# Performance work log

Measured on AMD Instinct MI355X. Metric: run time of the kernel, lower is better.

## Reference

```python
import jax, jax.numpy as jnp
import numpy as np

GRID_MIN, GRID_MAX, NUM_GRIDS = -2.0, 2.0, 8
DENOM = (GRID_MAX - GRID_MIN) / (NUM_GRIDS - 1)
DIM, NUM_HEADS = 768, 12
B, N = 8, 1024


def _layer_norm(x, w, b, eps=1e-5):
    mu = jnp.mean(x, axis=-1, keepdims=True)
    var = jnp.mean((x - mu) ** 2, axis=-1, keepdims=True)
    return (x - mu) * jax.lax.rsqrt(var + eps) * w + b


def _fastkan(x, ln_w, ln_b, spline_w, base_w, base_b):
    # x: [..., C]; spline_w: [C*G, O]; base_w: [C, O]
    grid = jnp.linspace(GRID_MIN, GRID_MAX, NUM_GRIDS, dtype=x.dtype)
    h = _layer_norm(x, ln_w, ln_b)
    # RBF basis expansion: [..., C, G]
    basis = jnp.exp(-(((h[..., None] - grid) / DENOM) ** 2))
    basis = basis.reshape(*basis.shape[:-2], -1)  # [..., C*G]
    ret = basis @ spline_w
    ret = ret + jax.nn.silu(x) @ base_w + base_b
    return ret


def setup_inputs() -> dict:
    key = jax.random.key(0)
    ks = jax.random.split(key, 6)
    C = DIM
    return {
        "x": jax.random.normal(ks[0], (B, N, C), jnp.float32),
        "qkv_ln_w": jnp.ones((C,), jnp.float32),
        "qkv_ln_b": jnp.zeros((C,), jnp.float32),
        "qkv_spline_w": jax.random.normal(ks[1], (C * NUM_GRIDS, 3 * C), jnp.float32) * 0.1,
        "qkv_base_w": jax.random.normal(ks[2], (C, 3 * C), jnp.float32) * (1.0 / np.sqrt(C)),
        "qkv_base_b": jnp.zeros((3 * C,), jnp.float32),
        "proj_ln_w": jnp.ones((C,), jnp.float32),
        "proj_ln_b": jnp.zeros((C,), jnp.float32),
        "proj_spline_w": jax.random.normal(ks[3], (C * NUM_GRIDS, C), jnp.float32) * 0.1,
        "proj_base_w": jax.random.normal(ks[4], (C, C), jnp.float32) * (1.0 / np.sqrt(C)),
        "proj_base_b": jnp.zeros((C,), jnp.float32),
    }


def reference(x, qkv_ln_w, qkv_ln_b, qkv_spline_w, qkv_base_w, qkv_base_b,
              proj_ln_w, proj_ln_b, proj_spline_w, proj_base_w, proj_base_b):
    b, n, c = x.shape
    h = NUM_HEADS
    d = c // h
    scale = d ** -0.5
    qkv = _fastkan(x, qkv_ln_w, qkv_ln_b, qkv_spline_w, qkv_base_w, qkv_base_b)
    qkv = qkv.reshape(b, n, 3, h, d).transpose(2, 0, 3, 1, 4)  # [3,B,H,N,D]
    q, k, v = qkv[0], qkv[1], qkv[2]
    attn = jnp.einsum("bhnd,bhmd->bhnm", q, k) * scale
    attn = jax.nn.softmax(attn, axis=-1)
    out = jnp.einsum("bhnm,bhmd->bhnd", attn, v)
    out = out.transpose(0, 2, 1, 3).reshape(b, n, c)
    out = _fastkan(out, proj_ln_w, proj_ln_b, proj_spline_w, proj_base_w, proj_base_b)
    return out
```

## Files before the change

kernel.cpp:

```cpp
#include <hip/hip_runtime.h>
#include <cstdint>
#include <cstddef>

typedef _Float16 h8 __attribute__((ext_vector_type(8)));
typedef float f4 __attribute__((ext_vector_type(4)));
typedef float f16f __attribute__((ext_vector_type(16)));

#define DEV static __device__ __forceinline__

DEV void gld16(const void* g, void* l) {
  __builtin_amdgcn_global_load_lds(
      (const __attribute__((address_space(1))) void*)g,
      (__attribute__((address_space(3))) void*)l, 16, 0, 0);
}

__global__ __launch_bounds__(256)
void kan_prep(const float* __restrict__ X, const float* __restrict__ lnw,
              const float* __restrict__ lnb, _Float16* __restrict__ Acat) {
  const int row = blockIdx.x;
  const int tid = threadIdx.x;
  const float* xr = X + (size_t)row * 768;
  float xv[3];
  xv[0] = xr[tid]; xv[1] = xr[tid + 256]; xv[2] = xr[tid + 512];
  float s = xv[0] + xv[1] + xv[2];
  float q = xv[0] * xv[0] + xv[1] * xv[1] + xv[2] * xv[2];
#pragma unroll
  for (int off = 32; off; off >>= 1) {
    s += __shfl_xor(s, off);
    q += __shfl_xor(q, off);
  }
  __shared__ float rs_[4], rq_[4];
  const int wave = tid >> 6;
  if ((tid & 63) == 0) { rs_[wave] = s; rq_[wave] = q; }
  __syncthreads();
  s = rs_[0] + rs_[1] + rs_[2] + rs_[3];
  q = rq_[0] + rq_[1] + rq_[2] + rq_[3];
  const float mu = s * (1.0f / 768.0f);
  const float var = q * (1.0f / 768.0f) - mu * mu;
  const float rsig = rsqrtf(var + 1e-5f);
  _Float16* out = Acat + (size_t)row * 6912;
#pragma unroll
  for (int i = 0; i < 3; ++i) {
    const int c = tid + i * 256;
    const float x = xv[i];
    const float h = (x - mu) * rsig * lnw[c] + lnb[c];
    union { h8 v; _Float16 u[8]; } bs;
#pragma unroll
    for (int g = 0; g < 8; ++g) {
      const float gv = -2.0f + (4.0f / 7.0f) * (float)g;
      const float t = (h - gv) * 1.75f;
      bs.u[g] = (_Float16)__expf(-t * t);
    }
    *(h8*)(out + c * 8) = bs.v;
    out[6144 + c] = (_Float16)(x / (1.0f + __expf(-x)));
  }
}

__global__ __launch_bounds__(256)
void wt_cast(const float* __restrict__ W, _Float16* __restrict__ Bp,
             int N, int koff, int nkt) {
  __shared__ float t[32][33];
  const int k0 = blockIdx.x * 32, n0 = blockIdx.y * 32;
  const int tx = threadIdx.x & 31, ty = threadIdx.x >> 5;
#pragma unroll
  for (int i = 0; i < 4; ++i)
    t[ty + i * 8][tx] = W[(size_t)(k0 + ty + i * 8) * N + n0 + tx];
  __syncthreads();
  const int f = threadIdx.x;
  if (f < 128) {
    const int nn = f & 31, cc = f >> 5;
    union { h8 v; _Float16 u[8]; } bs;
#pragma unroll
    for (int j = 0; j < 8; ++j) bs.u[j] = (_Float16)t[cc * 8 + j][nn];
    const int kg = koff + k0 + cc * 8;
    const int nt = (n0 + nn) >> 5;
    const size_t addr = ((size_t)nt * nkt + (kg >> 6)) * 2048 +
                        (size_t)((((kg >> 4) & 3) * 64 + nn + 32 * ((kg >> 3) & 1))) * 8;
    *(h8*)(Bp + addr) = bs.v;
  }
}

__global__ __launch_bounds__(256)
void v_transpose(const _Float16* __restrict__ qkv, _Float16* __restrict__ Vt) {
  const int bh = blockIdx.z, hh = bh % 12, b = bh / 12;
  const int kvb = blockIdx.x * 32, db = blockIdx.y * 32;
  __shared__ _Float16 t[32][33];
  const int tx = threadIdx.x & 31, ty = threadIdx.x >> 5;
#pragma unroll
  for (int i = 0; i < 4; ++i) {
    const int kv = kvb + ty + i * 8;
    t[ty + i * 8][tx] = qkv[(size_t)(b * 1024 + kv) * 2304 + 1536 + hh * 64 + db + tx];
  }
  __syncthreads();
#pragma unroll
  for (int i = 0; i < 4; ++i) {
    const int d = db + ty + i * 8;
    Vt[(size_t)(bh * 64 + d) * 1024 + kvb + tx] = t[tx][ty + i * 8];
  }
}

#define LOAD_B(dst)                                       \
  {                                                       \
    _Pragma("unroll") for (int ni = 0; ni < 2; ++ni) {    \
      _Pragma("unroll") for (int ks = 0; ks < 4; ++ks)    \
        dst[ni][ks] = *(const h8*)(bpp[ni] + ks * 512);   \
      bpp[ni] += 2048;                                    \
    }                                                     \
  }
#define LOAD_A(buf)                                       \
  {                                                       \
    _Pragma("unroll") for (int i = 0; i < 4; ++i) {       \
      gld16(ap[i], (buf) + alOff[i]);                     \
      ap[i] += 64;                                        \
    }                                                     \
  }
#define MFMA_STEP(buf, br)                                \
  {                                                       \
    const h8* A8 = (const h8*)(buf);                      \
    _Pragma("unroll") for (int ks = 0; ks < 4; ++ks) {    \
      const int o = (ks * 2 + half) ^ swz;                \
      h8 af0 = A8[(wm + l31) * 8 + o];                    \
      h8 af1 = A8[(wm + 32 + l31) * 8 + o];               \
      acc[0][0] = __builtin_amdgcn_mfma_f32_32x32x16_f16(af0, br[0][ks], acc[0][0], 0, 0, 0); \
      acc[0][1] = __builtin_amdgcn_mfma_f32_32x32x16_f16(af0, br[1][ks], acc[0][1], 0, 0, 0); \
      acc[1][0] = __builtin_amdgcn_mfma_f32_32x32x16_f16(af1, br[0][ks], acc[1][0], 0, 0, 0); \
      acc[1][1] = __builtin_amdgcn_mfma_f32_32x32x16_f16(af1, br[1][ks], acc[1][1], 0, 0, 0); \
    }                                                     \
  }

template <bool F16OUT>
__global__ __launch_bounds__(256, 2)
void gemm_bt(const _Float16* __restrict__ A, const _Float16* __restrict__ Bp,
             const float* __restrict__ bias, void* __restrict__ Cout,
             int N, int ldK, int kLen, size_t sliceStride) {
  __shared__ __align__(16) _Float16 As[2 * 128 * 64];
  _Float16* As0 = As;
  _Float16* As1 = As + 128 * 64;
  const int tid = threadIdx.x;
  const int lane = tid & 63, wave = tid >> 6;
  const int gx = gridDim.x;
  const int lin = blockIdx.y * gx + blockIdx.x;
  const int xcd = lin & 7, pos = lin >> 3;
  const int bandH = gridDim.y >> 3;
  const int bm = (xcd * bandH + pos / gx) * 128;
  const int bn = (pos % gx) * 128;
  const int slice = blockIdx.z;
  const int kOff = slice * kLen;
  const int rsub = lane >> 3;
  const int l7 = lane & 7;
  const int l31 = lane & 31, half = lane >> 5;
  const int wm = (wave >> 1) * 64, wn = (wave & 1) * 64;
  const _Float16* ap[4];
  int alOff[4];
#pragma unroll
  for (int i = 0; i < 4; ++i) {
    const int ch = wave * 4 + i;
    const int ksw = (l7 ^ rsub ^ ((ch & 3) << 1)) * 8;
    ap[i] = A + (size_t)(bm + ch * 8 + rsub) * ldK + kOff + ksw;
    alOff[i] = ch * 512;
  }
  const size_t nktTot = (size_t)(ldK >> 6);
  const int kt0 = kOff >> 6;
  const _Float16* bpp[2];
#pragma unroll
  for (int ni = 0; ni < 2; ++ni)
    bpp[ni] = Bp + ((size_t)((bn >> 5) + (wn >> 5) + ni) * nktTot + kt0) * 2048 + lane * 8;

  f16f acc[2][2] = {};
  const int swz = l7 ^ ((rsub & 3) << 1);
  const int nkt = kLen >> 6;
  h8 bregA[2][4], bregB[2][4];
  LOAD_B(bregA);
  LOAD_A(As0);
  for (int kt = 0; kt < nkt; kt += 2) {
    __syncthreads();
    if (kt + 1 < nkt) { LOAD_B(bregB); LOAD_A(As1); }
    MFMA_STEP(As0, bregA);
    __syncthreads();
    if (kt + 2 < nkt) { LOAD_B(bregA); LOAD_A(As0); }
    MFMA_STEP(As1, bregB);
  }
#pragma unroll
  for (int ni = 0; ni < 2; ++ni) {
    const int col = bn + wn + ni * 32 + l31;
    const float bv = bias ? bias[col] : 0.0f;
#pragma unroll
    for (int mi = 0; mi < 2; ++mi) {
      const int rb = bm + wm + mi * 32 + 4 * half;
#pragma unroll
      for (int reg = 0; reg < 16; ++reg) {
        const int r = rb + (reg & 3) + 8 * (reg >> 2);
        const float v = acc[mi][ni][reg] + bv;
        if (F16OUT)
          ((_Float16*)Cout)[(size_t)r * N + col] = (_Float16)v;
        else
          ((float*)Cout + slice * sliceStride)[(size_t)r * N + col] = v;
      }
    }
  }
}

__global__ __launch_bounds__(256)
void attn(const _Float16* __restrict__ qkv, const _Float16* __restrict__ Vt,
          float* __restrict__ ctx) {
  __shared__ __align__(16) _Float16 Qs[128 * 64];
  __shared__ __align__(16) _Float16 Ks[64 * 64];
  __shared__ __align__(16) _Float16 Vs[64 * 64];
  __shared__ __align__(16) _Float16 Ps[4 * 32 * 72];
  const int tid = threadIdx.x;
  const int lane = tid & 63, wave = tid >> 6;
  const int bh = blockIdx.y, hh = bh % 12, b = bh / 12;
  const int qt = blockIdx.x;
  const int rsub = lane >> 3;
  const int ksw = ((lane & 7) ^ rsub) * 8;
#pragma unroll
  for (int i = 0; i < 4; ++i) {
    const int ch = wave * 4 + i;
    const int row = ch * 8 + rsub;
    gld16(qkv + (size_t)(b * 1024 + qt * 128 + row) * 2304 + hh * 64 + ksw, Qs + ch * 512);
  }
  const int l16 = lane & 15, quad = lane >> 4, r7 = l16 & 7;
  f4 acc_o[2][4] = {};
  float m_old[2][4], l_sum[2][4];
#pragma unroll
  for (int mi = 0; mi < 2; ++mi)
#pragma unroll
    for (int j = 0; j < 4; ++j) { m_old[mi][j] = -1e30f; l_sum[mi][j] = 0.0f; }

  _Float16* Pw = Ps + wave * (32 * 72);

  for (int kv0 = 0; kv0 < 1024; kv0 += 64) {
#pragma unroll
    for (int i = 0; i < 2; ++i) {
      const int ch = wave * 2 + i;
      const int row = ch * 8 + rsub;
      gld16(qkv + (size_t)(b * 1024 + kv0 + row) * 2304 + 768 + hh * 64 + ksw, Ks + ch * 512);
      gld16(Vt + (size_t)(bh * 64 + row) * 1024 + kv0 + ksw, Vs + ch * 512);
    }
    __syncthreads();
    const h8* Q8 = (const h8*)Qs;
    const h8* K8 = (const h8*)Ks;
    const h8* V8 = (const h8*)Vs;
    f4 s[2][4] = {};
#pragma unroll
    for (int ks = 0; ks < 2; ++ks) {
      const int kq = (ks * 4 + quad) ^ r7;
      h8 qf[2], kf[4];
#pragma unroll
      for (int mi = 0; mi < 2; ++mi) qf[mi] = Q8[(wave * 32 + mi * 16 + l16) * 8 + kq];
#pragma unroll
      for (int ni = 0; ni < 4; ++ni) kf[ni] = K8[(ni * 16 + l16) * 8 + kq];
#pragma unroll
      for (int mi = 0; mi < 2; ++mi)
#pragma unroll
        for (int ni = 0; ni < 4; ++ni)
          s[mi][ni] = __builtin_amdgcn_mfma_f32_16x16x32_f16(qf[mi], kf[ni], s[mi][ni], 0, 0, 0);
    }
#pragma unroll
    for (int mi = 0; mi < 2; ++mi)
#pragma unroll
      for (int ni = 0; ni < 4; ++ni) s[mi][ni] *= 0.125f;
#pragma unroll
    for (int mi = 0; mi < 2; ++mi) {
#pragma unroll
      for (int j = 0; j < 4; ++j) {
        float vm = fmaxf(fmaxf(s[mi][0][j], s[mi][1][j]), fmaxf(s[mi][2][j], s[mi][3][j]));
#pragma unroll
        for (int off = 1; off < 16; off <<= 1) vm = fmaxf(vm, __shfl_xor(vm, off));
        const float mn = fmaxf(m_old[mi][j], vm);
        const float alpha = __expf(m_old[mi][j] - mn);
        float rs = 0.0f;
#pragma unroll
        for (int ni = 0; ni < 4; ++ni) {
          const float p = __expf(s[mi][ni][j] - mn);
          s[mi][ni][j] = p;
          rs += p;
        }
#pragma unroll
        for (int off = 1; off < 16; off <<= 1) rs += __shfl_xor(rs, off);
        l_sum[mi][j] = l_sum[mi][j] * alpha + rs;
        m_old[mi][j] = mn;
#pragma unroll
        for (int ni = 0; ni < 4; ++ni) acc_o[mi][ni][j] *= alpha;
      }
    }
#pragma unroll
    for (int mi = 0; mi < 2; ++mi)
#pragma unroll
      for (int ni = 0; ni < 4; ++ni)
#pragma unroll
        for (int j = 0; j < 4; ++j)
          Pw[(mi * 16 + quad * 4 + j) * 72 + ni * 16 + l16] = (_Float16)s[mi][ni][j];
#pragma unroll
    for (int ks = 0; ks < 2; ++ks) {
      const int kq = ks * 4 + quad;
      h8 pf[2], vf[4];
#pragma unroll
      for (int mi = 0; mi < 2; ++mi) pf[mi] = *(const h8*)(Pw + (mi * 16 + l16) * 72 + kq * 8);
#pragma unroll
      for (int ni = 0; ni < 4; ++ni) vf[ni] = V8[(ni * 16 + l16) * 8 + (kq ^ r7)];
#pragma unroll
      for (int mi = 0; mi < 2; ++mi)
#pragma unroll
        for (int ni = 0; ni < 4; ++ni)
          acc_o[mi][ni] = __builtin_amdgcn_mfma_f32_16x16x32_f16(pf[mi], vf[ni], acc_o[mi][ni], 0, 0, 0);
    }
    __syncthreads();
  }
#pragma unroll
  for (int mi = 0; mi < 2; ++mi) {
#pragma unroll
    for (int j = 0; j < 4; ++j) {
      const float inv = 1.0f / l_sum[mi][j];
      const int tok = b * 1024 + qt * 128 + wave * 32 + mi * 16 + quad * 4 + j;
      float* cr = ctx + (size_t)tok * 768 + hh * 64;
#pragma unroll
      for (int ni = 0; ni < 4; ++ni) cr[ni * 16 + l16] = acc_o[mi][ni][j] * inv;
    }
  }
}

extern "C" void kernel_launch(void* const* d_in, const int* in_sizes, int n_in,
                              void* d_out, int out_size, void* d_ws, size_t ws_size,
                              hipStream_t stream) {
  (void)in_sizes; (void)n_in; (void)out_size; (void)ws_size;
  const float* x    = (const float*)d_in[0];
  const float* qlnw = (const float*)d_in[1];
  const float* qlnb = (const float*)d_in[2];
  const float* qsw  = (const float*)d_in[3];
  const float* qbw  = (const float*)d_in[4];
  const float* qbb  = (const float*)d_in[5];
  const float* plnw = (const float*)d_in[6];
  const float* plnb = (const float*)d_in[7];
  const float* psw  = (const float*)d_in[8];
  const float* pbw  = (const float*)d_in[9];
  const float* pbb  = (const float*)d_in[10];
  float* out = (float*)d_out;

  _Float16* WtQ  = (_Float16*)d_ws;
  _Float16* WtP  = WtQ + (size_t)2304 * 6912;
  _Float16* Acat = WtP + (size_t)768 * 6912;
  _Float16* QKV  = Acat + (size_t)8192 * 6912;
  _Float16* Vt   = QKV + (size_t)8192 * 2304;
  float* CTX = (float*)(Vt + (size_t)96 * 64 * 1024);

  dim3 blk(256);
  wt_cast<<<dim3(192, 72), blk, 0, stream>>>(qsw, WtQ, 2304, 0, 108);
  wt_cast<<<dim3(24, 72),  blk, 0, stream>>>(qbw, WtQ, 2304, 6144, 108);
  wt_cast<<<dim3(192, 24), blk, 0, stream>>>(psw, WtP, 768, 0, 108);
  wt_cast<<<dim3(24, 24),  blk, 0, stream>>>(pbw, WtP, 768, 6144, 108);
  kan_prep<<<8192, blk, 0, stream>>>(x, qlnw, qlnb, Acat);
  gemm_bt<true><<<dim3(2304 / 128, 8192 / 128, 1), blk, 0, stream>>>(
      Acat, WtQ, qbb, QKV, 2304, 6912, 6912, 0);
  v_transpose<<<dim3(32, 2, 96), blk, 0, stream>>>(QKV, Vt);
  attn<<<dim3(8, 96), blk, 0, stream>>>(QKV, Vt, CTX);
  kan_prep<<<8192, blk, 0, stream>>>(CTX, plnw, plnb, Acat);
  gemm_bt<false><<<dim3(768 / 128, 8192 / 128, 1), blk, 0, stream>>>(
      Acat, WtP, pbb, out, 768, 6912, 6912, 0);
}
```

Baseline: 717.0 us.

## Use 256x128 tile GEMM with XCD-aware block mapping for QKV projection

Adds a new GEMM kernel for the QKV KAN projection that computes 256x128 output tiles per block, with 4x2 MFMA tiles per wave, double-buffered A tiles in LDS and B held in registers. Blocks are remapped so each XCD processes a contiguous band of M rows, which is meant to improve L2 reuse of the A and B operands. The larger tile halves B reloads per output and raises arithmetic intensity. The cost is more accumulator registers and 64KB of LDS per block, which may reduce occupancy.

```diff
diff --git a/kernel.cpp b/kernel.cpp
--- a/kernel.cpp
+++ b/kernel.cpp
@@ -200,6 +200,89 @@
   }
 }
 
+__global__ __launch_bounds__(256, 2)
+void gemm_bt2(const _Float16* __restrict__ A, const _Float16* __restrict__ Bp,
+              const float* __restrict__ bias, _Float16* __restrict__ Cout,
+              int N, int ldK) {
+  __shared__ __align__(16) _Float16 As[2 * 256 * 64];
+  _Float16* As0 = As;
+  _Float16* As1 = As + 256 * 64;
+  const int tid = threadIdx.x;
+  const int lane = tid & 63, wave = tid >> 6;
+  const int gx = gridDim.x;
+  const int lin = blockIdx.y * gx + blockIdx.x;
+  const int xcd = lin & 7, pos = lin >> 3;
+  const int bandH = gridDim.y >> 3;
+  const int bm = (xcd * bandH + pos / gx) * 256;
+  const int bn = (pos % gx) * 128;
+  const int rsub = lane >> 3;
+  const int l7 = lane & 7;
+  const int l31 = lane & 31, half = lane >> 5;
+  const int wm = (wave >> 1) * 128, wn = (wave & 1) * 64;
+  const _Float16* ap[8];
+  int alOff[8];
+#pragma unroll
+  for (int i = 0; i < 8; ++i) {
+    const int ch = wave * 8 + i;
+    const int ksw = (l7 ^ rsub ^ ((ch & 3) << 1)) * 8;
+    ap[i] = A + (size_t)(bm + ch * 8 + rsub) * ldK + ksw;
+    alOff[i] = ch * 512;
+  }
+  const size_t nktTot = (size_t)(ldK >> 6);
+  const _Float16* bpp[2];
+#pragma unroll
+  for (int ni = 0; ni < 2; ++ni)
+    bpp[ni] = Bp + (size_t)((bn >> 5) + (wn >> 5) + ni) * nktTot * 2048 + lane * 8;
+
+  f16f acc[4][2] = {};
+  const int swz = l7 ^ ((rsub & 3) << 1);
+  const int nkt = ldK >> 6;
+  h8 bregA[2][4], bregB[2][4];
+#define LOAD_A2(buf)                                      \
+  {                                                       \
+    _Pragma("unroll") for (int i = 0; i < 8; ++i) {       \
+      gld16(ap[i], (buf) + alOff[i]);                     \
+      ap[i] += 64;                                        \
+    }                                                     \
+  }
+#define MFMA_STEP2(buf, br)                               \
+  {                                                       \
+    const h8* A8 = (const h8*)(buf);                      \
+    _Pragma("unroll") for (int ks = 0; ks < 4; ++ks) {    \
+      const int o = (ks * 2 + half) ^ swz;                \
+      _Pragma("unroll") for (int mi = 0; mi < 4; ++mi) {  \
+        h8 af = A8[(wm + mi * 32 + l31) * 8 + o];         \
+        acc[mi][0] = __builtin_amdgcn_mfma_f32_32x32x16_f16(af, br[0][ks], acc[mi][0], 0, 0, 0); \
+        acc[mi][1] = __builtin_amdgcn_mfma_f32_32x32x16_f16(af, br[1][ks], acc[mi][1], 0, 0, 0); \
+      }                                                   \
+    }                                                     \
+  }
+  LOAD_B(bregA);
+  LOAD_A2(As0);
+  for (int kt = 0; kt < nkt; kt += 2) {
+    __syncthreads();
+    if (kt + 1 < nkt) { LOAD_B(bregB); LOAD_A2(As1); }
+    MFMA_STEP2(As0, bregA);
+    __syncthreads();
+    if (kt + 2 < nkt) { LOAD_B(bregA); LOAD_A2(As0); }
+    MFMA_STEP2(As1, bregB);
+  }
+#pragma unroll
+  for (int ni = 0; ni < 2; ++ni) {
+    const int col = bn + wn + ni * 32 + l31;
+    const float bv = bias[col];
+#pragma unroll
+    for (int mi = 0; mi < 4; ++mi) {
+      const int rb = bm + wm + mi * 32 + 4 * half;
+#pragma unroll
+      for (int reg = 0; reg < 16; ++reg) {
+        const int r = rb + (reg & 3) + 8 * (reg >> 2);
+        Cout[(size_t)r * N + col] = (_Float16)(acc[mi][ni][reg] + bv);
+      }
+    }
+  }
+}
+
 __global__ __launch_bounds__(256)
 void attn(const _Float16* __restrict__ qkv, const _Float16* __restrict__ Vt,
           float* __restrict__ ctx) {
@@ -350,8 +433,8 @@
   wt_cast<<<dim3(192, 24), blk, 0, stream>>>(psw, WtP, 768, 0, 108);
   wt_cast<<<dim3(24, 24),  blk, 0, stream>>>(pbw, WtP, 768, 6144, 108);
   kan_prep<<<8192, blk, 0, stream>>>(x, qlnw, qlnb, Acat);
-  gemm_bt<true><<<dim3(2304 / 128, 8192 / 128, 1), blk, 0, stream>>>(
-      Acat, WtQ, qbb, QKV, 2304, 6912, 6912, 0);
+  gemm_bt2<<<dim3(2304 / 128, 8192 / 256), blk, 0, stream>>>(
+      Acat, WtQ, qbb, QKV, 2304, 6912);
   v_transpose<<<dim3(32, 2, 96), blk, 0, stream>>>(QKV, Vt);
   attn<<<dim3(8, 96), blk, 0, stream>>>(QKV, Vt, CTX);
   kan_prep<<<8192, blk, 0, stream>>>(CTX, plnw, plnb, Acat);
```

Result: slower. 733.5 us (+2.3%).

## Enlarge attention KV tile to 128, keep Q in registers, fold scale into exp

Applied to the files above, without the earlier changes.

The attention kernel now loads each wave's Q fragments straight into registers instead of staging them through shared memory. The KV tile grows from 64 to 128 keys per iteration, which halves the number of barrier-synchronised loop trips. The 0.125 scale is folded into the exponent argument, and s_setprio hints are wrapped around the MFMA sections. In exchange the kernel uses more score registers and a new V swizzle layout, which may lower occupancy.

```diff
diff --git a/kernel.cpp b/kernel.cpp
--- a/kernel.cpp
+++ b/kernel.cpp
@@ -203,23 +203,26 @@
 __global__ __launch_bounds__(256)
 void attn(const _Float16* __restrict__ qkv, const _Float16* __restrict__ Vt,
           float* __restrict__ ctx) {
-  __shared__ __align__(16) _Float16 Qs[128 * 64];
-  __shared__ __align__(16) _Float16 Ks[64 * 64];
-  __shared__ __align__(16) _Float16 Vs[64 * 64];
+  __shared__ __align__(16) _Float16 Ks[128 * 64];
+  __shared__ __align__(16) _Float16 Vs[64 * 128];
   __shared__ __align__(16) _Float16 Ps[4 * 32 * 72];
   const int tid = threadIdx.x;
   const int lane = tid & 63, wave = tid >> 6;
   const int bh = blockIdx.y, hh = bh % 12, b = bh / 12;
   const int qt = blockIdx.x;
   const int rsub = lane >> 3;
-  const int ksw = ((lane & 7) ^ rsub) * 8;
-#pragma unroll
-  for (int i = 0; i < 4; ++i) {
-    const int ch = wave * 4 + i;
-    const int row = ch * 8 + rsub;
-    gld16(qkv + (size_t)(b * 1024 + qt * 128 + row) * 2304 + hh * 64 + ksw, Qs + ch * 512);
-  }
+  const int l7 = lane & 7;
+  const int ksw = (l7 ^ rsub) * 8;
   const int l16 = lane & 15, quad = lane >> 4, r7 = l16 & 7;
+  const int l15 = lane & 15, q4 = lane >> 4;
+  h8 qreg[2][2];
+#pragma unroll
+  for (int mi = 0; mi < 2; ++mi)
+#pragma unroll
+    for (int ks = 0; ks < 2; ++ks) {
+      const size_t row = (size_t)(b * 1024 + qt * 128 + wave * 32 + mi * 16 + l16);
+      qreg[mi][ks] = *(const h8*)(qkv + row * 2304 + hh * 64 + (ks * 4 + quad) * 8);
+    }
   f4 acc_o[2][4] = {};
   float m_old[2][4], l_sum[2][4];
 #pragma unroll
@@ -229,50 +232,55 @@
 
   _Float16* Pw = Ps + wave * (32 * 72);
 
-  for (int kv0 = 0; kv0 < 1024; kv0 += 64) {
-#pragma unroll
-    for (int i = 0; i < 2; ++i) {
-      const int ch = wave * 2 + i;
+  for (int it = 0; it < 8; ++it) {
+    const int kv0 = it * 128;
+#pragma unroll
+    for (int i = 0; i < 4; ++i) {
+      const int ch = wave * 4 + i;
       const int row = ch * 8 + rsub;
-      gld16(qkv + (size_t)(b * 1024 + kv0 + row) * 2304 + 768 + hh * 64 + ksw, Ks + ch * 512);
-      gld16(Vt + (size_t)(bh * 64 + row) * 1024 + kv0 + ksw, Vs + ch * 512);
+      gld16(qkv + (size_t)(b * 1024 + kv0 + row) * 2304 + 768 + hh * 64 + ksw,
+            Ks + ch * 512);
+    }
+#pragma unroll
+    for (int i = 0; i < 4; ++i) {
+      const int chv = wave * 4 + i;
+      const int d = chv * 4 + q4;
+      const int csw = l15 ^ (d & 7);
+      gld16(Vt + (size_t)(bh * 64 + d) * 1024 + kv0 + csw * 8, Vs + chv * 512);
     }
     __syncthreads();
-    const h8* Q8 = (const h8*)Qs;
     const h8* K8 = (const h8*)Ks;
     const h8* V8 = (const h8*)Vs;
-    f4 s[2][4] = {};
+    f4 s[2][8] = {};
+    __builtin_amdgcn_s_setprio(1);
 #pragma unroll
     for (int ks = 0; ks < 2; ++ks) {
       const int kq = (ks * 4 + quad) ^ r7;
-      h8 qf[2], kf[4];
-#pragma unroll
-      for (int mi = 0; mi < 2; ++mi) qf[mi] = Q8[(wave * 32 + mi * 16 + l16) * 8 + kq];
-#pragma unroll
-      for (int ni = 0; ni < 4; ++ni) kf[ni] = K8[(ni * 16 + l16) * 8 + kq];
+      h8 kf[8];
+#pragma unroll
+      for (int ni = 0; ni < 8; ++ni) kf[ni] = K8[(ni * 16 + l16) * 8 + kq];
 #pragma unroll
       for (int mi = 0; mi < 2; ++mi)
 #pragma unroll
-        for (int ni = 0; ni < 4; ++ni)
-          s[mi][ni] = __builtin_amdgcn_mfma_f32_16x16x32_f16(qf[mi], kf[ni], s[mi][ni], 0, 0, 0);
-    }
-#pragma unroll
-    for (int mi = 0; mi < 2; ++mi)
-#pragma unroll
-      for (int ni = 0; ni < 4; ++ni) s[mi][ni] *= 0.125f;
+        for (int ni = 0; ni < 8; ++ni)
+          s[mi][ni] = __builtin_amdgcn_mfma_f32_16x16x32_f16(qreg[mi][ks], kf[ni], s[mi][ni], 0, 0, 0);
+    }
+    __builtin_amdgcn_s_setprio(0);
 #pragma unroll
     for (int mi = 0; mi < 2; ++mi) {
 #pragma unroll
       for (int j = 0; j < 4; ++j) {
-        float vm = fmaxf(fmaxf(s[mi][0][j], s[mi][1][j]), fmaxf(s[mi][2][j], s[mi][3][j]));
+        float vm = s[mi][0][j];
+#pragma unroll
+        for (int ni = 1; ni < 8; ++ni) vm = fmaxf(vm, s[mi][ni][j]);
 #pragma unroll
         for (int off = 1; off < 16; off <<= 1) vm = fmaxf(vm, __shfl_xor(vm, off));
         const float mn = fmaxf(m_old[mi][j], vm);
-        const float alpha = __expf(m_old[mi][j] - mn);
+        const float alpha = __expf((m_old[mi][j] - mn) * 0.125f);
         float rs = 0.0f;
 #pragma unroll
-        for (int ni = 0; ni < 4; ++ni) {
-          const float p = __expf(s[mi][ni][j] - mn);
+        for (int ni = 0; ni < 8; ++ni) {
+          const float p = __expf((s[mi][ni][j] - mn) * 0.125f);
           s[mi][ni][j] = p;
           rs += p;
         }
@@ -285,25 +293,33 @@
       }
     }
 #pragma unroll
-    for (int mi = 0; mi < 2; ++mi)
-#pragma unroll
-      for (int ni = 0; ni < 4; ++ni)
-#pragma unroll
-        for (int j = 0; j < 4; ++j)
-          Pw[(mi * 16 + quad * 4 + j) * 72 + ni * 16 + l16] = (_Float16)s[mi][ni][j];
-#pragma unroll
-    for (int ks = 0; ks < 2; ++ks) {
-      const int kq = ks * 4 + quad;
-      h8 pf[2], vf[4];
-#pragma unroll
-      for (int mi = 0; mi < 2; ++mi) pf[mi] = *(const h8*)(Pw + (mi * 16 + l16) * 72 + kq * 8);
-#pragma unroll
-      for (int ni = 0; ni < 4; ++ni) vf[ni] = V8[(ni * 16 + l16) * 8 + (kq ^ r7)];
+    for (int hf = 0; hf < 2; ++hf) {
 #pragma unroll
       for (int mi = 0; mi < 2; ++mi)
 #pragma unroll
         for (int ni = 0; ni < 4; ++ni)
-          acc_o[mi][ni] = __builtin_amdgcn_mfma_f32_16x16x32_f16(pf[mi], vf[ni], acc_o[mi][ni], 0, 0, 0);
+#pragma unroll
+          for (int j = 0; j < 4; ++j)
+            Pw[(mi * 16 + quad * 4 + j) * 72 + ni * 16 + l16] =
+                (_Float16)s[mi][hf * 4 + ni][j];
+      __builtin_amdgcn_s_setprio(1);
+#pragma unroll
+      for (int ks = 0; ks < 2; ++ks) {
+        const int kq = hf * 8 + ks * 4 + quad;
+        h8 pf[2], vf[4];
+#pragma unroll
+        for (int mi = 0; mi < 2; ++mi)
+          pf[mi] = *(const h8*)(Pw + (mi * 16 + l16) * 72 + (ks * 4 + quad) * 8);
+#pragma unroll
+        for (int nd = 0; nd < 4; ++nd)
+          vf[nd] = V8[(nd * 16 + l16) * 16 + (kq ^ r7)];
+#pragma unroll
+        for (int mi = 0; mi < 2; ++mi)
+#pragma unroll
+          for (int nd = 0; nd < 4; ++nd)
+            acc_o[mi][nd] = __builtin_amdgcn_mfma_f32_16x16x32_f16(pf[mi], vf[nd], acc_o[mi][nd], 0, 0, 0);
+      }
+      __builtin_amdgcn_s_setprio(0);
     }
     __syncthreads();
   }
```

Result: slower. 733.4 us (+2.3%).

## Double-buffer K tiles in attention, read V directly from global, add setprio

Applied to the files above, without the earlier changes.

The attention kernel now double-buffers K tiles in shared memory, prefetching the next tile while computing the current one, with a single barrier per iteration. V fragments are loaded straight from global memory into registers instead of being staged through LDS. s_setprio is raised around the MFMA sections. This aims to hide K load latency and cut LDS traffic and one barrier per iteration, at the cost of uncoalesced, unshared global reads of V across waves, which may add latency on the PV path.

```diff
diff --git a/kernel.cpp b/kernel.cpp
--- a/kernel.cpp
+++ b/kernel.cpp
@@ -204,8 +204,7 @@
 void attn(const _Float16* __restrict__ qkv, const _Float16* __restrict__ Vt,
           float* __restrict__ ctx) {
   __shared__ __align__(16) _Float16 Qs[128 * 64];
-  __shared__ __align__(16) _Float16 Ks[64 * 64];
-  __shared__ __align__(16) _Float16 Vs[64 * 64];
+  __shared__ __align__(16) _Float16 Ks[2][64 * 64];
   __shared__ __align__(16) _Float16 Ps[4 * 32 * 72];
   const int tid = threadIdx.x;
   const int lane = tid & 63, wave = tid >> 6;
@@ -219,6 +218,12 @@
     const int row = ch * 8 + rsub;
     gld16(qkv + (size_t)(b * 1024 + qt * 128 + row) * 2304 + hh * 64 + ksw, Qs + ch * 512);
   }
+#pragma unroll
+  for (int i = 0; i < 2; ++i) {
+    const int ch = wave * 2 + i;
+    const int row = ch * 8 + rsub;
+    gld16(qkv + (size_t)(b * 1024 + row) * 2304 + 768 + hh * 64 + ksw, Ks[0] + ch * 512);
+  }
   const int l16 = lane & 15, quad = lane >> 4, r7 = l16 & 7;
   f4 acc_o[2][4] = {};
   float m_old[2][4], l_sum[2][4];
@@ -228,20 +233,26 @@
     for (int j = 0; j < 4; ++j) { m_old[mi][j] = -1e30f; l_sum[mi][j] = 0.0f; }
 
   _Float16* Pw = Ps + wave * (32 * 72);
-
-  for (int kv0 = 0; kv0 < 1024; kv0 += 64) {
-#pragma unroll
-    for (int i = 0; i < 2; ++i) {
-      const int ch = wave * 2 + i;
-      const int row = ch * 8 + rsub;
-      gld16(qkv + (size_t)(b * 1024 + kv0 + row) * 2304 + 768 + hh * 64 + ksw, Ks + ch * 512);
-      gld16(Vt + (size_t)(bh * 64 + row) * 1024 + kv0 + ksw, Vs + ch * 512);
-    }
-    __syncthreads();
+  const _Float16* vbase = Vt + (size_t)bh * 64 * 1024;
+
+  for (int it = 0; it < 16; ++it) {
+    const int kv0 = it * 64;
+    asm volatile("s_waitcnt vmcnt(0) lgkmcnt(0)" ::: "memory");
+    __builtin_amdgcn_s_barrier();
+    if (it < 15) {
+      const int kvn = kv0 + 64;
+#pragma unroll
+      for (int i = 0; i < 2; ++i) {
+        const int ch = wave * 2 + i;
+        const int row = ch * 8 + rsub;
+        gld16(qkv + (size_t)(b * 1024 + kvn + row) * 2304 + 768 + hh * 64 + ksw,
+              Ks[(it + 1) & 1] + ch * 512);
+      }
+    }
     const h8* Q8 = (const h8*)Qs;
-    const h8* K8 = (const h8*)Ks;
-    const h8* V8 = (const h8*)Vs;
+    const h8* K8 = (const h8*)Ks[it & 1];
     f4 s[2][4] = {};
+    __builtin_amdgcn_s_setprio(1);
 #pragma unroll
     for (int ks = 0; ks < 2; ++ks) {
       const int kq = (ks * 4 + quad) ^ r7;
@@ -256,6 +267,7 @@
         for (int ni = 0; ni < 4; ++ni)
           s[mi][ni] = __builtin_amdgcn_mfma_f32_16x16x32_f16(qf[mi], kf[ni], s[mi][ni], 0, 0, 0);
     }
+    __builtin_amdgcn_s_setprio(0);
 #pragma unroll
     for (int mi = 0; mi < 2; ++mi)
 #pragma unroll
@@ -291,6 +303,7 @@
 #pragma unroll
         for (int j = 0; j < 4; ++j)
           Pw[(mi * 16 + quad * 4 + j) * 72 + ni * 16 + l16] = (_Float16)s[mi][ni][j];
+    __builtin_amdgcn_s_setprio(1);
 #pragma unroll
     for (int ks = 0; ks < 2; ++ks) {
       const int kq = ks * 4 + quad;
@@ -298,14 +311,15 @@
 #pragma unroll
       for (int mi = 0; mi < 2; ++mi) pf[mi] = *(const h8*)(Pw + (mi * 16 + l16) * 72 + kq * 8);
 #pragma unroll
-      for (int ni = 0; ni < 4; ++ni) vf[ni] = V8[(ni * 16 + l16) * 8 + (kq ^ r7)];
+      for (int ni = 0; ni < 4; ++ni)
+        vf[ni] = *(const h8*)(vbase + (size_t)(ni * 16 + l16) * 1024 + kv0 + kq * 8);
 #pragma unroll
       for (int mi = 0; mi < 2; ++mi)
 #pragma unroll
         for (int ni = 0; ni < 4; ++ni)
           acc_o[mi][ni] = __builtin_amdgcn_mfma_f32_16x16x32_f16(pf[mi], vf[ni], acc_o[mi][ni], 0, 0, 0);
     }
-    __syncthreads();
+    __builtin_amdgcn_s_setprio(0);
   }
 #pragma unroll
   for (int mi = 0; mi < 2; ++mi) {
```

Result: no change. 718.4 us (+0.2%).
